# Performance work log

Hardware: AMD Instinct MI355X
Metric: run time of the kernel (lower is better)

## Reference

```python
import jax, jax.numpy as jnp
import numpy as np

EPS = 1e-5
HEADS = 16
GROUPS = 16


def _bn(x, gamma, beta, mean, var, ch_axis):
    # eval-mode batchnorm along channel axis
    shape = [1] * x.ndim
    shape[ch_axis] = -1
    scale = gamma / jnp.sqrt(var + EPS)
    return (x - mean.reshape(shape)) * scale.reshape(shape) + beta.reshape(shape)


def setup_inputs() -> dict:
    key = jax.random.key(0)
    ks = jax.random.split(key, 20)
    N, Ct, L = 2, 256, 256
    Cf, Co = 256, 256
    H = W = 128
    G, Cg = GROUPS, Cf // GROUPS  # 16, 16
    nrm = lambda k, sh, s=1.0: (jax.random.normal(k, sh, jnp.float32) * s)
    return {
        "feature": nrm(ks[0], (N, Cf, H, W)),
        "tokens": nrm(ks[1], (N, Ct, L)),
        "w_v": nrm(ks[2], (Co, Ct), 1.0 / np.sqrt(Ct)),
        "b_v": nrm(ks[3], (Co,), 0.05),
        "g_v": 1.0 + nrm(ks[4], (Co,), 0.1),
        "be_v": nrm(ks[5], (Co,), 0.05),
        "m_v": nrm(ks[6], (Co,), 0.05),
        "v_v": 0.5 + jax.random.uniform(ks[7], (Co,), jnp.float32),
        "w_k": nrm(ks[8], (Cf, Ct), 1.0 / np.sqrt(Ct)),
        "b_k": nrm(ks[9], (Cf,), 0.05),
        "g_k": 1.0 + nrm(ks[10], (Cf,), 0.1),
        "be_k": nrm(ks[11], (Cf,), 0.05),
        "m_k": nrm(ks[12], (Cf,), 0.05),
        "v_k": 0.5 + jax.random.uniform(ks[13], (Cf,), jnp.float32),
        "w_q": nrm(ks[14], (G, Cg, Cg), 1.0 / np.sqrt(Cg)),  # grouped 1x1 conv
        "b_q": nrm(ks[15], (Cf,), 0.05),
        "g_q": 1.0 + nrm(ks[16], (Cf,), 0.1),
        "be_q": nrm(ks[17], (Cf,), 0.05),
        "m_q": nrm(ks[18], (Cf,), 0.05),
        "v_q": 0.5 + jax.random.uniform(ks[19], (Cf,), jnp.float32),
    }


def reference(feature, tokens, w_v, b_v, g_v, be_v, m_v, v_v,
              w_k, b_k, g_k, be_k, m_k, v_k,
              w_q, b_q, g_q, be_q, m_q, v_q):
    N, Ct, L = tokens.shape
    _, Cf, H, W = feature.shape
    h = HEADS
    # value / key: 1x1 conv1d + BN1d over channel axis 1
    pv = _bn(jnp.einsum('oc,ncl->nol', w_v, tokens) + b_v[:, None],
             g_v, be_v, m_v, v_v, 1)  # [N, Co, L]
    pk = _bn(jnp.einsum('oc,ncl->nol', w_k, tokens) + b_k[:, None],
             g_k, be_k, m_k, v_k, 1)  # [N, Cf, L]
    # query: grouped 1x1 conv2d + BN
    G = GROUPS
    fg = feature.reshape(N, G, Cf // G, H, W)
    pq = jnp.einsum('goc,ngchw->ngohw', w_q, fg).reshape(N, Cf, H, W)
    pq = _bn(pq + b_q[None, :, None, None], g_q, be_q, m_q, v_q, 1)
    # multi-head cross attention
    dq = Cf // h  # head dim = 16
    q = pq.reshape(N, h, dq, H * W)        # [N,h,d,S]
    k = pk.reshape(N, h, dq, L)            # [N,h,d,L]
    v = pv.reshape(N, h, -1, L)            # [N,h,dv,L]
    scores = jnp.einsum('nhds,nhdl->nhsl', q, k) / jnp.sqrt(jnp.float32(dq))
    coef = jax.nn.softmax(scores, axis=-1)  # softmax over tokens L
    proj = jnp.einsum('nhvl,nhsl->nhvs', v, coef).reshape(N, -1, H, W)
    # out_channels == feature_channels -> lateral_conv is None
    return feature + proj
```

## Files before the change

kernel.cpp:

```cpp
#include <hip/hip_runtime.h>
#include <hip/hip_bf16.h>
#include <math.h>

#define EPSV 1e-5f
#define LOG2E 1.4426950408889634f

typedef short short8v __attribute__((ext_vector_type(8)));
typedef __bf16 bf16x8 __attribute__((ext_vector_type(8)));
typedef float f32x4 __attribute__((ext_vector_type(4)));

__device__ __forceinline__ float bsu2f(unsigned short u) {
    union { unsigned int i; float f; } x; x.i = ((unsigned int)u) << 16; return x.f;
}
__device__ __forceinline__ float ldf(const void* p, int i, int isbf) {
    return isbf ? bsu2f(((const unsigned short*)p)[i]) : ((const float*)p)[i];
}
__device__ __forceinline__ short f2bs(float x) {
    __hip_bfloat16 h = __float2bfloat16(x);
    return *reinterpret_cast<short*>(&h);
}
__device__ __forceinline__ int packbf(short a, short b) {
    return (int)(unsigned short)a | ((int)(unsigned short)b << 16);
}
__device__ __forceinline__ int permpack(unsigned int hi, unsigned int lo) {
    return (int)__builtin_amdgcn_perm(hi, lo, 0x07060302u);
}
__device__ __forceinline__ unsigned int fbits_rhu(float x) {
    return __float_as_uint(x) + 0x8000u;
}
__device__ __forceinline__ int probe_bf16(const void* vv) {
    const unsigned short* p = (const unsigned short*)vv;
    int cnt = 0;
#pragma unroll
    for (int i = 0; i < 16; ++i) {
        const float x = bsu2f(p[i]);
        cnt += (x >= 0.01f && x <= 100.0f) ? 1 : 0;
    }
    return cnt >= 14;
}

__global__ __launch_bounds__(256) void prep_kernel(
    const void* __restrict__ tokens,
    const void* __restrict__ w_v, const void* __restrict__ b_v,
    const void* __restrict__ g_v, const void* __restrict__ be_v,
    const void* __restrict__ m_v, const void* __restrict__ v_v,
    const void* __restrict__ w_k, const void* __restrict__ b_k,
    const void* __restrict__ g_k, const void* __restrict__ be_k,
    const void* __restrict__ m_k, const void* __restrict__ v_k,
    int* __restrict__ ka, int* __restrict__ va, int* __restrict__ flag)
{
    __shared__ __align__(16) short Wh[16][264];
    __shared__ __align__(16) short Tt[256][40];
    __shared__ float scs[16], shs[16];

    const int tid = threadIdx.x;
    const int h = blockIdx.x, kv = blockIdx.y, n = blockIdx.z;
    const int isbf = probe_bf16(v_v);
    if (h == 0 && kv == 0 && n == 0 && tid == 0) *flag = isbf;

    const void* w  = kv ? w_k  : w_v;
    const void* b  = kv ? b_k  : b_v;
    const void* g  = kv ? g_k  : g_v;
    const void* be = kv ? be_k : be_v;
    const void* mm = kv ? m_k  : m_v;
    const void* vv = kv ? v_k  : v_v;

    {
        const int d = tid >> 4, c0 = (tid & 15) * 16;
        const int off = (h * 16 + d) * 256 + c0;
        if (isbf) {
            const unsigned short* ws = (const unsigned short*)w + off;
#pragma unroll
            for (int i = 0; i < 16; ++i) Wh[d][c0 + i] = (short)ws[i];
        } else {
            const float* ws = (const float*)w + off;
#pragma unroll
            for (int i = 0; i < 16; ++i) Wh[d][c0 + i] = f2bs(ws[i]);
        }
    }
    if (tid < 16) {
        const int ch = h * 16 + tid;
        const float s = ldf(g, ch, isbf) * rsqrtf(ldf(vv, ch, isbf) + EPSV);
        scs[tid] = s;
        shs[tid] = (ldf(b, ch, isbf) - ldf(mm, ch, isbf)) * s + ldf(be, ch, isbf);
    }

    const int lane = tid & 63, w_ = tid >> 6;
    const int q = lane >> 4, p = lane & 15;

    f32x4 acc[4];
    const f32x4 zero = {0.f, 0.f, 0.f, 0.f};
#pragma unroll
    for (int t = 0; t < 4; ++t) acc[t] = zero;

    for (int ch8 = 0; ch8 < 8; ++ch8) {
        const int c0 = ch8 * 32;
        __syncthreads();
#pragma unroll
        for (int p2 = 0; p2 < 2; ++p2) {
            const int ccl = p2 * 16 + (tid >> 5) * 2;
            const int cc = c0 + ccl;
            const int l0 = (tid & 31) * 8;
            if (isbf) {
                const unsigned short* tp = (const unsigned short*)tokens + n * 65536;
                const int4 r0 = *(const int4*)(tp + cc * 256 + l0);
                const int4 r1 = *(const int4*)(tp + (cc + 1) * 256 + l0);
                const unsigned short* a = (const unsigned short*)&r0;
                const unsigned short* bb = (const unsigned short*)&r1;
#pragma unroll
                for (int i = 0; i < 8; ++i)
                    *(int*)&Tt[l0 + i][ccl] = (int)a[i] | ((int)bb[i] << 16);
            } else {
                const float* tp = (const float*)tokens + n * 65536;
#pragma unroll
                for (int i = 0; i < 8; ++i) {
                    const int aa = (int)(unsigned short)f2bs(tp[cc * 256 + l0 + i]);
                    const int bb = (int)(unsigned short)f2bs(tp[(cc + 1) * 256 + l0 + i]);
                    *(int*)&Tt[l0 + i][ccl] = aa | (bb << 16);
                }
            }
        }
        __syncthreads();
        const short8v wf = *(const short8v*)&Wh[p][c0 + q * 8];
#pragma unroll
        for (int t = 0; t < 4; ++t) {
            const int l = (w_ * 4 + t) * 16 + p;
            const short8v tf = *(const short8v*)&Tt[l][q * 8];
            if (kv)
                acc[t] = __builtin_amdgcn_mfma_f32_16x16x32_bf16(
                    __builtin_bit_cast(bf16x8, wf), __builtin_bit_cast(bf16x8, tf),
                    acc[t], 0, 0, 0);
            else
                acc[t] = __builtin_amdgcn_mfma_f32_16x16x32_bf16(
                    __builtin_bit_cast(bf16x8, tf), __builtin_bit_cast(bf16x8, wf),
                    acc[t], 0, 0, 0);
        }
    }

    if (kv) {
        float sc4[4], sh4[4];
#pragma unroll
        for (int r = 0; r < 4; ++r) { sc4[r] = scs[q * 4 + r]; sh4[r] = shs[q * 4 + r]; }
        const int qs = ((q & 1) << 1) | (q >> 1);
        int* dst_nh = ka + (n * 16 + h) * 2048;
#pragma unroll
        for (int t = 0; t < 4; ++t) {
            const int tau = w_ * 4 + t;
            const int T = (tau >> 1) * 2 + ((p >> 2) & 1);
            const int m = ((tau & 1) * 2 + (p >> 3)) * 4 + (p & 3);
            const int L = (qs >> 1) * 16 + m;
            int* dst = dst_nh + (T * 32 + L) * 4 + (qs & 1) * 2;
            dst[0] = packbf(f2bs(fmaf(acc[t][0], sc4[0], sh4[0])),
                            f2bs(fmaf(acc[t][1], sc4[1], sh4[1])));
            dst[1] = packbf(f2bs(fmaf(acc[t][2], sc4[2], sh4[2])),
                            f2bs(fmaf(acc[t][3], sc4[3], sh4[3])));
        }
    } else {
        const float scp = scs[p], shp = shs[p];
        int* dst_nh = va + (n * 16 + h) * 2048;
#pragma unroll
        for (int t = 0; t < 4; ++t) {
            const int tau = w_ * 4 + t;
            const int c = tau >> 1;
            const int L = ((tau & 1) * 2 + (q >> 1)) * 16 + p;
            int* dst = dst_nh + (c * 64 + L) * 4 + (q & 1) * 2;
            dst[0] = packbf(f2bs(fmaf(acc[t][0], scp, shp)),
                            f2bs(fmaf(acc[t][1], scp, shp)));
            dst[1] = packbf(f2bs(fmaf(acc[t][2], scp, shp)),
                            f2bs(fmaf(acc[t][3], scp, shp)));
        }
    }
}

__global__ __launch_bounds__(256) void attn_kernel(
    const void* __restrict__ feature,
    const int* __restrict__ ka_g, const int* __restrict__ va_g,
    const void* __restrict__ w_q, const void* __restrict__ b_q,
    const void* __restrict__ g_q, const void* __restrict__ be_q,
    const void* __restrict__ m_q, const void* __restrict__ v_q,
    const int* __restrict__ flag, void* __restrict__ out)
{
    __shared__ __align__(16) short KAsh[16][32][8];
    __shared__ __align__(16) short VAsh[8][64][8];
    __shared__ __align__(16) short Wqsh[16][24];
    __shared__ __align__(16) float Bqsh[16];
    __shared__ __align__(16) float Osh[16][64];

    const int tid = threadIdx.x;
    const int bx = blockIdx.x, h = blockIdx.y, n = blockIdx.z;
    const int isbf = *flag;

    {
        const int4* kas = (const int4*)ka_g + (n * 16 + h) * 512;
        const int4* vas = (const int4*)va_g + (n * 16 + h) * 512;
#pragma unroll
        for (int k = 0; k < 2; ++k) {
            const int slot = k * 256 + tid;
            ((int4*)KAsh)[slot] = kas[slot];
            ((int4*)VAsh)[slot] = vas[slot];
        }
        const int d = tid >> 4, ch = h * 16 + d;
        const float aqd = 0.25f * LOG2E *
                          ldf(g_q, ch, isbf) * rsqrtf(ldf(v_q, ch, isbf) + EPSV);
        Wqsh[d][tid & 15] = f2bs(ldf(w_q, h * 256 + tid, isbf) * aqd);
        if (tid < 16) {
            const int c2 = h * 16 + tid;
            const float sq = ldf(g_q, c2, isbf) * rsqrtf(ldf(v_q, c2, isbf) + EPSV);
            Bqsh[tid] = 0.25f * LOG2E *
                        ((ldf(b_q, c2, isbf) - ldf(m_q, c2, isbf)) * sq + ldf(be_q, c2, isbf));
        }
    }
    __syncthreads();

    const int lane = tid & 63, w_ = tid >> 6;
    const int q = lane >> 4, p = lane & 15;
    const f32x4 zero = {0.f, 0.f, 0.f, 0.f};

    const int px = bx * 64 + w_ * 16 + p;
    const int fbase = n * 4194304 + (h * 16) * 16384 + px;
    int4 fpack = {0, 0, 0, 0};
    if (q < 2) {
        const int c0 = q * 8;
        if (isbf) {
            const unsigned short* fp = (const unsigned short*)feature + fbase + c0 * 16384;
            unsigned int u[8];
#pragma unroll
            for (int j = 0; j < 8; ++j) u[j] = fp[j * 16384];
            fpack.x = (int)(u[0] | (u[1] << 16));
            fpack.y = (int)(u[2] | (u[3] << 16));
            fpack.z = (int)(u[4] | (u[5] << 16));
            fpack.w = (int)(u[6] | (u[7] << 16));
        } else {
            const float* fp = (const float*)feature + fbase + c0 * 16384;
            fpack.x = packbf(f2bs(fp[0]), f2bs(fp[16384]));
            fpack.y = packbf(f2bs(fp[2 * 16384]), f2bs(fp[3 * 16384]));
            fpack.z = packbf(f2bs(fp[4 * 16384]), f2bs(fp[5 * 16384]));
            fpack.w = packbf(f2bs(fp[6 * 16384]), f2bs(fp[7 * 16384]));
        }
    }
    const short8v waf = *(const short8v*)&Wqsh[p][(q & 1) * 8];
    f32x4 qc = __builtin_amdgcn_mfma_f32_16x16x32_bf16(
        __builtin_bit_cast(bf16x8, waf), __builtin_bit_cast(bf16x8, fpack),
        zero, 0, 0, 0);
    const f32x4 bq4 = *(const f32x4*)&Bqsh[q * 4];
    unsigned int a0 = fbits_rhu(qc[0] + bq4[0]);
    unsigned int a1 = fbits_rhu(qc[1] + bq4[1]);
    unsigned int a2 = fbits_rhu(qc[2] + bq4[2]);
    unsigned int a3 = fbits_rhu(qc[3] + bq4[3]);
    const unsigned int o0 = (unsigned int)__shfl_xor((int)a0, 32, 64);
    const unsigned int o1 = (unsigned int)__shfl_xor((int)a1, 32, 64);
    const unsigned int o2 = (unsigned int)__shfl_xor((int)a2, 32, 64);
    const unsigned int o3 = (unsigned int)__shfl_xor((int)a3, 32, 64);
    int4 qp = {0, 0, 0, 0};
    if (q < 2) {
        qp.x = permpack(a1, a0);
        qp.y = permpack(a3, a2);
        qp.z = permpack(o1, o0);
        qp.w = permpack(o3, o2);
    }
    const bf16x8 qbb = __builtin_bit_cast(bf16x8, qp);

    f32x4 S[16];
#pragma unroll
    for (int T = 0; T < 16; ++T) {
        const short8v kaf = *(const short8v*)&KAsh[T][lane & 31][0];
        S[T] = __builtin_amdgcn_mfma_f32_16x16x32_bf16(
            __builtin_bit_cast(bf16x8, kaf), qbb, zero, 0, 0, 0);
    }

    float ssum = 0.f;
#pragma unroll
    for (int T = 0; T < 16; ++T)
#pragma unroll
        for (int r = 0; r < 4; ++r) {
            const float e = exp2f(S[T][r]);
            S[T][r] = e;
            ssum += e;
        }
    ssum += __shfl_xor(ssum, 16, 64);
    ssum += __shfl_xor(ssum, 32, 64);
    const float inv = 1.0f / ssum;

    f32x4 oacc = zero;
#pragma unroll
    for (int c = 0; c < 8; ++c) {
        const unsigned int u0 = fbits_rhu(S[2 * c][0]), u1 = fbits_rhu(S[2 * c][1]);
        const unsigned int u2 = fbits_rhu(S[2 * c][2]), u3 = fbits_rhu(S[2 * c][3]);
        const unsigned int v0 = fbits_rhu(S[2 * c + 1][0]), v1 = fbits_rhu(S[2 * c + 1][1]);
        const unsigned int v2 = fbits_rhu(S[2 * c + 1][2]), v3 = fbits_rhu(S[2 * c + 1][3]);
        int4 pbp;
        pbp.x = permpack(u1, u0);
        pbp.y = permpack(u3, u2);
        pbp.z = permpack(v1, v0);
        pbp.w = permpack(v3, v2);
        const short8v vaf = *(const short8v*)&VAsh[c][lane][0];
        oacc = __builtin_amdgcn_mfma_f32_16x16x32_bf16(
            __builtin_bit_cast(bf16x8, vaf), __builtin_bit_cast(bf16x8, pbp),
            oacc, 0, 0, 0);
    }

#pragma unroll
    for (int r = 0; r < 4; ++r) Osh[q * 4 + r][w_ * 16 + p] = oacc[r] * inv;
    __syncthreads();

    {
        const int pxe = tid & 63;
        const int base2 = n * 4194304 + (h * 16) * 16384 + bx * 64 + pxe;
        if (isbf) {
            const unsigned short* fp = (const unsigned short*)feature;
            __hip_bfloat16* op = (__hip_bfloat16*)out;
#pragma unroll
            for (int r = 0; r < 4; ++r) {
                const int ch = r * 4 + w_;
                const int idx = base2 + ch * 16384;
                op[idx] = __float2bfloat16(Osh[ch][pxe] + bsu2f(fp[idx]));
            }
        } else {
            const float* fp = (const float*)feature;
            float* op = (float*)out;
#pragma unroll
            for (int r = 0; r < 4; ++r) {
                const int ch = r * 4 + w_;
                const int idx = base2 + ch * 16384;
                op[idx] = Osh[ch][pxe] + fp[idx];
            }
        }
    }
}

extern "C" void kernel_launch(void* const* d_in, const int* in_sizes, int n_in,
                              void* d_out, int out_size, void* d_ws, size_t ws_size,
                              hipStream_t stream) {
    const void* feature = d_in[0];
    const void* tokens  = d_in[1];
    const void* w_v  = d_in[2];  const void* b_v  = d_in[3];
    const void* g_v  = d_in[4];  const void* be_v = d_in[5];
    const void* m_v  = d_in[6];  const void* v_v  = d_in[7];
    const void* w_k  = d_in[8];  const void* b_k  = d_in[9];
    const void* g_k  = d_in[10]; const void* be_k = d_in[11];
    const void* m_k  = d_in[12]; const void* v_k  = d_in[13];
    const void* w_q  = d_in[14]; const void* b_q  = d_in[15];
    const void* g_q  = d_in[16]; const void* be_q = d_in[17];
    const void* m_q  = d_in[18]; const void* v_q  = d_in[19];

    int* ka = (int*)d_ws;
    int* va = ka + 65536;
    int* flag = va + 65536;

    prep_kernel<<<dim3(16, 2, 2), 256, 0, stream>>>(
        tokens, w_v, b_v, g_v, be_v, m_v, v_v,
        w_k, b_k, g_k, be_k, m_k, v_k, ka, va, flag);
    attn_kernel<<<dim3(256, 16, 2), 256, 0, stream>>>(
        feature, ka, va, w_q, b_q, g_q, be_q, m_q, v_q, flag, (void*)d_out);
}
```

Before: 182.2 us.

## Fold query bias into MFMA, use raw exp/rcp, write output directly from registers

The query bias is folded into the grouped-conv MFMA by adding a constant-one input lane and placing the bias as an extra weight column, which removes the separate bias loads and adds. The softmax uses the hardware exp2 and reciprocal intrinsics and sums with vector adds. The shared-memory output staging and its second block barrier are removed, so each lane adds the residual and stores straight from the MFMA accumulator. The direct stores are strided per lane, which may coalesce worse than the staged layout, and the bias is now rounded to bf16.

```diff
diff --git a/kernel.cpp b/kernel.cpp
--- a/kernel.cpp
+++ b/kernel.cpp
@@ -27,6 +27,23 @@
 }
 __device__ __forceinline__ unsigned int fbits_rhu(float x) {
     return __float_as_uint(x) + 0x8000u;
+}
+__device__ __forceinline__ unsigned short rhu16(float x) {
+    return (unsigned short)((__float_as_uint(x) + 0x8000u) >> 16);
+}
+__device__ __forceinline__ float rexp2(float x) {
+#if __has_builtin(__builtin_amdgcn_exp2f)
+    return __builtin_amdgcn_exp2f(x);
+#else
+    float r; asm("v_exp_f32 %0, %1" : "=v"(r) : "v"(x)); return r;
+#endif
+}
+__device__ __forceinline__ float frcp(float x) {
+#if __has_builtin(__builtin_amdgcn_rcpf)
+    return __builtin_amdgcn_rcpf(x);
+#else
+    return 1.0f / x;
+#endif
 }
 __device__ __forceinline__ int probe_bf16(const void* vv) {
     const unsigned short* p = (const unsigned short*)vv;
@@ -182,9 +199,7 @@
 {
     __shared__ __align__(16) short KAsh[16][32][8];
     __shared__ __align__(16) short VAsh[8][64][8];
-    __shared__ __align__(16) short Wqsh[16][24];
-    __shared__ __align__(16) float Bqsh[16];
-    __shared__ __align__(16) float Osh[16][64];
+    __shared__ __align__(16) short Wqsh[16][32];
 
     const int tid = threadIdx.x;
     const int bx = blockIdx.x, h = blockIdx.y, n = blockIdx.z;
@@ -203,11 +218,16 @@
         const float aqd = 0.25f * LOG2E *
                           ldf(g_q, ch, isbf) * rsqrtf(ldf(v_q, ch, isbf) + EPSV);
         Wqsh[d][tid & 15] = f2bs(ldf(w_q, h * 256 + tid, isbf) * aqd);
+        if (tid < 128) {
+            const int row = tid >> 3, j = tid & 7;
+            if (j) *(int*)&Wqsh[row][16 + j * 2] = 0;
+        }
         if (tid < 16) {
             const int c2 = h * 16 + tid;
             const float sq = ldf(g_q, c2, isbf) * rsqrtf(ldf(v_q, c2, isbf) + EPSV);
-            Bqsh[tid] = 0.25f * LOG2E *
-                        ((ldf(b_q, c2, isbf) - ldf(m_q, c2, isbf)) * sq + ldf(be_q, c2, isbf));
+            const float bq = 0.25f * LOG2E *
+                ((ldf(b_q, c2, isbf) - ldf(m_q, c2, isbf)) * sq + ldf(be_q, c2, isbf));
+            *(int*)&Wqsh[tid][16] = (int)(unsigned short)f2bs(bq);
         }
     }
     __syncthreads();
@@ -237,16 +257,17 @@
             fpack.z = packbf(f2bs(fp[4 * 16384]), f2bs(fp[5 * 16384]));
             fpack.w = packbf(f2bs(fp[6 * 16384]), f2bs(fp[7 * 16384]));
         }
-    }
-    const short8v waf = *(const short8v*)&Wqsh[p][(q & 1) * 8];
+    } else if (q == 2) {
+        fpack.x = 0x3F80;
+    }
+    const short8v waf = *(const short8v*)&Wqsh[p][q * 8];
     f32x4 qc = __builtin_amdgcn_mfma_f32_16x16x32_bf16(
         __builtin_bit_cast(bf16x8, waf), __builtin_bit_cast(bf16x8, fpack),
         zero, 0, 0, 0);
-    const f32x4 bq4 = *(const f32x4*)&Bqsh[q * 4];
-    unsigned int a0 = fbits_rhu(qc[0] + bq4[0]);
-    unsigned int a1 = fbits_rhu(qc[1] + bq4[1]);
-    unsigned int a2 = fbits_rhu(qc[2] + bq4[2]);
-    unsigned int a3 = fbits_rhu(qc[3] + bq4[3]);
+    unsigned int a0 = fbits_rhu(qc[0]);
+    unsigned int a1 = fbits_rhu(qc[1]);
+    unsigned int a2 = fbits_rhu(qc[2]);
+    unsigned int a3 = fbits_rhu(qc[3]);
     const unsigned int o0 = (unsigned int)__shfl_xor((int)a0, 32, 64);
     const unsigned int o1 = (unsigned int)__shfl_xor((int)a1, 32, 64);
     const unsigned int o2 = (unsigned int)__shfl_xor((int)a2, 32, 64);
@@ -268,18 +289,17 @@
             __builtin_bit_cast(bf16x8, kaf), qbb, zero, 0, 0, 0);
     }
 
-    float ssum = 0.f;
-#pragma unroll
-    for (int T = 0; T < 16; ++T)
-#pragma unroll
-        for (int r = 0; r < 4; ++r) {
-            const float e = exp2f(S[T][r]);
-            S[T][r] = e;
-            ssum += e;
-        }
+    f32x4 ssum4 = zero;
+#pragma unroll
+    for (int T = 0; T < 16; ++T) {
+#pragma unroll
+        for (int r = 0; r < 4; ++r) S[T][r] = rexp2(S[T][r]);
+        ssum4 += S[T];
+    }
+    float ssum = (ssum4[0] + ssum4[1]) + (ssum4[2] + ssum4[3]);
     ssum += __shfl_xor(ssum, 16, 64);
     ssum += __shfl_xor(ssum, 32, 64);
-    const float inv = 1.0f / ssum;
+    const float inv = frcp(ssum);
 
     f32x4 oacc = zero;
 #pragma unroll
@@ -299,31 +319,22 @@
             oacc, 0, 0, 0);
     }
 
-#pragma unroll
-    for (int r = 0; r < 4; ++r) Osh[q * 4 + r][w_ * 16 + p] = oacc[r] * inv;
-    __syncthreads();
-
-    {
-        const int pxe = tid & 63;
-        const int base2 = n * 4194304 + (h * 16) * 16384 + bx * 64 + pxe;
-        if (isbf) {
-            const unsigned short* fp = (const unsigned short*)feature;
-            __hip_bfloat16* op = (__hip_bfloat16*)out;
-#pragma unroll
-            for (int r = 0; r < 4; ++r) {
-                const int ch = r * 4 + w_;
-                const int idx = base2 + ch * 16384;
-                op[idx] = __float2bfloat16(Osh[ch][pxe] + bsu2f(fp[idx]));
-            }
-        } else {
-            const float* fp = (const float*)feature;
-            float* op = (float*)out;
-#pragma unroll
-            for (int r = 0; r < 4; ++r) {
-                const int ch = r * 4 + w_;
-                const int idx = base2 + ch * 16384;
-                op[idx] = Osh[ch][pxe] + fp[idx];
-            }
+    const int obase = n * 4194304 + (h * 16 + q * 4) * 16384 + px;
+    if (isbf) {
+        const unsigned short* fp = (const unsigned short*)feature;
+        unsigned short* op = (unsigned short*)out;
+#pragma unroll
+        for (int r = 0; r < 4; ++r) {
+            const int idx = obase + r * 16384;
+            op[idx] = rhu16(fmaf(oacc[r], inv, bsu2f(fp[idx])));
+        }
+    } else {
+        const float* fp = (const float*)feature;
+        float* op = (float*)out;
+#pragma unroll
+        for (int r = 0; r < 4; ++r) {
+            const int idx = obase + r * 16384;
+            op[idx] = fmaf(oacc[r], inv, fp[idx]);
         }
     }
 }
```

Measured after the change: 172.6 us. 5.2% less time.
